# Kernel tuning notes

Measured on AMD Instinct MI355X. Metric: run time of the kernel, lower is better.

The kernel has to match this reference:

```python
import jax, jax.numpy as jnp
import numpy as np

T, B, C, S = 4096, 8, 512, 2048


def setup_inputs() -> dict:
    key = jax.random.key(0)
    k1, k2, k3 = jax.random.split(key, 3)
    x = jax.random.normal(k1, (T, B, C), dtype=jnp.float32)
    downsampling_mask = jax.random.uniform(k2, (B, T, S), dtype=jnp.float32)
    size_of_groups = jax.random.randint(k3, (B, S), 0, 4, dtype=jnp.int64)
    leftmost_group = jnp.zeros((1, 1, C), dtype=jnp.float32)
    return {"x": x, "downsampling_mask": downsampling_mask,
            "size_of_groups": size_of_groups, "leftmost_group": leftmost_group}


def reference(x, downsampling_mask, size_of_groups, leftmost_group):
    # mode == 'average': masked grouped pooling as a dense contraction
    # x: [T,B,C], mask: [B,T,S] -> downsampled: [S,B,C]
    downsampled = jnp.einsum('tbc,bts->sbc', x, downsampling_mask)
    # prepend learned leftmost group embedding, broadcast over batch
    left = jnp.broadcast_to(leftmost_group, (1, x.shape[1], x.shape[2]))
    return jnp.concatenate([left, downsampled], axis=0)  # [S+1, B, C]
```

## Files before the change

### kernel.cpp

```cpp
#include <hip/hip_runtime.h>
#include <hip/hip_bf16.h>

constexpr int T  = 4096;
constexpr int Bb = 8;
constexpr int C  = 512;
constexpr int S  = 2048;
constexpr int BC = Bb * C;

constexpr int BK = 64;
constexpr int NK = T / BK;

typedef __bf16 bf16x8 __attribute__((ext_vector_type(8)));
typedef float  f32x16 __attribute__((ext_vector_type(16)));
typedef float  f32x4  __attribute__((ext_vector_type(4)));

__device__ inline unsigned pk2(float lo, float hi) {
    union { __hip_bfloat16 h; unsigned short u; } a, b;
    a.h = __float2bfloat16(lo);
    b.h = __float2bfloat16(hi);
    return ((unsigned)b.u << 16) | (unsigned)a.u;
}

__device__ inline int slot16(int s) { return s ^ ((s >> 2) & 7); }

__global__ void left_fill(const float* __restrict__ left, float* __restrict__ out) {
    int i = blockIdx.x * blockDim.x + threadIdx.x;
    if (i < BC) out[i] = left[i & (C - 1)];
}

__global__ __launch_bounds__(512, 4) void ds_gemm(
    const float* __restrict__ x,
    const float* __restrict__ mask,
    float* __restrict__ out)
{
    __shared__ __align__(16) unsigned char smem[65536];

    const int bid0 = blockIdx.x;
    const int xcd  = bid0 & 7;
    const int slot = bid0 >> 3;
    const int b    = xcd;
    const int mt   = slot & 15;
    const int nt   = (slot >> 4) & 3;

    const int tid  = threadIdx.x;
    const int lane = tid & 63;
    const int wave = tid >> 6;
    const int h    = wave >> 2;
    const int wq   = wave & 3;
    const int wm = wq >> 1;
    const int wn = wq & 1;
    const int lm = lane & 31;
    const int kg = lane >> 5;

    const int  ii  = tid & 255;
    const int  sg  = ii & 31;
    const int  tg  = ii >> 5;
    const bool stB = (tid >= 256);

    const float* gsrc = stB
        ? x    + (size_t)(tg * 8) * BC + b * C + nt * 128 + sg * 4
        : mask + (size_t)b * T * S + (size_t)(tg * 8) * S + mt * 128 + sg * 4;
    const size_t grow  = stB ? (size_t)BC : (size_t)S;
    const size_t gstep = grow * BK;

    int waddr[4];
#pragma unroll
    for (int j = 0; j < 4; ++j)
        waddr[j] = (stB ? 16384 : 0) + tg * 2048 + slot16(sg * 4 + j) * 16;

    int raddrA[2][2], raddrB[2][2];
#pragma unroll
    for (int kk = 0; kk < 2; ++kk)
#pragma unroll
        for (int q = 0; q < 2; ++q) {
            const int oct = h * 4 + kk * 2 + kg;
            raddrA[kk][q] = oct * 2048 + slot16(wm * 64 + q * 32 + lm) * 16;
            raddrB[kk][q] = 16384 + oct * 2048 + slot16(wn * 64 + q * 32 + lm) * 16;
        }

    f32x16 acc[2][2] = {};
    f32x4  L[8];

#define LOAD_TILE(k)                                                        \
    {                                                                       \
        const float* p_ = gsrc + (size_t)(k) * gstep;                       \
        _Pragma("unroll") for (int r = 0; r < 8; ++r)                       \
            L[r] = *(const f32x4*)(p_ + (size_t)r * grow);                  \
    }

#define WRITE_TILE(buf)                                                     \
    {                                                                       \
        const int boff_ = (buf) * 32768;                                    \
        _Pragma("unroll") for (int j = 0; j < 4; ++j) {                     \
            uint4 w_;                                                       \
            w_.x = pk2(L[0][j], L[1][j]);                                   \
            w_.y = pk2(L[2][j], L[3][j]);                                   \
            w_.z = pk2(L[4][j], L[5][j]);                                   \
            w_.w = pk2(L[6][j], L[7][j]);                                   \
            *(uint4*)(smem + boff_ + waddr[j]) = w_;                        \
        }                                                                   \
    }

#define COMPUTE(buf)                                                        \
    {                                                                       \
        const int boff_ = (buf) * 32768;                                    \
        _Pragma("unroll") for (int kk = 0; kk < 2; ++kk) {                  \
            bf16x8 a0_ = *(const bf16x8*)(smem + boff_ + raddrA[kk][0]);    \
            bf16x8 a1_ = *(const bf16x8*)(smem + boff_ + raddrA[kk][1]);    \
            bf16x8 b0_ = *(const bf16x8*)(smem + boff_ + raddrB[kk][0]);    \
            bf16x8 b1_ = *(const bf16x8*)(smem + boff_ + raddrB[kk][1]);    \
            acc[0][0] = __builtin_amdgcn_mfma_f32_32x32x16_bf16(a0_, b0_, acc[0][0], 0, 0, 0); \
            acc[0][1] = __builtin_amdgcn_mfma_f32_32x32x16_bf16(a0_, b1_, acc[0][1], 0, 0, 0); \
            acc[1][0] = __builtin_amdgcn_mfma_f32_32x32x16_bf16(a1_, b0_, acc[1][0], 0, 0, 0); \
            acc[1][1] = __builtin_amdgcn_mfma_f32_32x32x16_bf16(a1_, b1_, acc[1][1], 0, 0, 0); \
        }                                                                   \
    }

    LOAD_TILE(0);

    for (int k = 0; k < NK; ++k) {
        WRITE_TILE(k & 1);
        if (k + 1 < NK) LOAD_TILE(k + 1);
        asm volatile("s_waitcnt lgkmcnt(0)" ::: "memory");
        __builtin_amdgcn_s_barrier();
        __builtin_amdgcn_sched_barrier(0);
        COMPUTE(k & 1);
    }

#undef LOAD_TILE
#undef WRITE_TILE
#undef COMPUTE

    __syncthreads();
    if (h == 1) {
#pragma unroll
        for (int m2 = 0; m2 < 2; ++m2)
#pragma unroll
            for (int n2 = 0; n2 < 2; ++n2) {
                unsigned char* base = smem + (wave - 4) * 16384 + (m2 * 2 + n2) * 4096 + lane * 16;
#pragma unroll
                for (int r4 = 0; r4 < 4; ++r4) {
                    f32x4 v = { acc[m2][n2][r4 * 4 + 0], acc[m2][n2][r4 * 4 + 1],
                                acc[m2][n2][r4 * 4 + 2], acc[m2][n2][r4 * 4 + 3] };
                    *(f32x4*)(base + r4 * 1024) = v;
                }
            }
    }
    __syncthreads();
    if (h == 0) {
#pragma unroll
        for (int m2 = 0; m2 < 2; ++m2)
#pragma unroll
            for (int n2 = 0; n2 < 2; ++n2) {
                const unsigned char* base = smem + wave * 16384 + (m2 * 2 + n2) * 4096 + lane * 16;
#pragma unroll
                for (int r4 = 0; r4 < 4; ++r4) {
                    f32x4 v = *(const f32x4*)(base + r4 * 1024);
#pragma unroll
                    for (int j = 0; j < 4; ++j) acc[m2][n2][r4 * 4 + j] += v[j];
                }
            }

        const int s_w = mt * 128 + wm * 64;
        const int c_w = nt * 128 + wn * 64;
        float* outp = out + BC;
#pragma unroll
        for (int m2 = 0; m2 < 2; ++m2)
#pragma unroll
            for (int n2 = 0; n2 < 2; ++n2)
#pragma unroll
                for (int r = 0; r < 16; ++r) {
                    const int row  = (r & 3) + 8 * (r >> 2) + 4 * kg;
                    const int srow = s_w + m2 * 32 + row;
                    const int ccol = c_w + n2 * 32 + lm;
                    outp[(size_t)srow * BC + b * C + ccol] = acc[m2][n2][r];
                }
    }
}

extern "C" void kernel_launch(void* const* d_in, const int* in_sizes, int n_in,
                              void* d_out, int out_size, void* d_ws, size_t ws_size,
                              hipStream_t stream) {
    const float* x    = (const float*)d_in[0];
    const float* mask = (const float*)d_in[1];
    const float* left = (const float*)d_in[3];
    float* out = (float*)d_out;

    left_fill<<<BC / 256, 256, 0, stream>>>(left, out);
    ds_gemm<<<Bb * (S / 128) * (C / 128), 512, 0, stream>>>(x, mask, out);
}
```

Before: 143.6 us.

## Interleave half-tile global loads and LDS writes with MFMA clusters

Restructures the main K loop so the next tile's global loads are issued before compute. Each K tile is split into two MFMA clusters, and each half of the next tile's LDS writes goes in after a partial vmcnt wait. The aim is to hide global-load latency and LDS write time behind MFMA work. It also raises wave priority around the MFMA issue with s_setprio. The cost is extra barriers per iteration (one inside each cluster plus the end-of-iteration one), more synchronisation overhead, and narrower uint2 LDS stores.

After: 155.6 us. 8.4% more time.

```diff
diff --git a/kernel.cpp b/kernel.cpp
--- a/kernel.cpp
+++ b/kernel.cpp
@@ -81,55 +81,75 @@
     f32x16 acc[2][2] = {};
     f32x4  L[8];
 
-#define LOAD_TILE(k)                                                        \
+#define LOAD_HALF(k, r0)                                                    \
     {                                                                       \
         const float* p_ = gsrc + (size_t)(k) * gstep;                       \
-        _Pragma("unroll") for (int r = 0; r < 8; ++r)                       \
-            L[r] = *(const f32x4*)(p_ + (size_t)r * grow);                  \
-    }
-
-#define WRITE_TILE(buf)                                                     \
+        _Pragma("unroll") for (int r = 0; r < 4; ++r)                       \
+            L[r0 + r] = *(const f32x4*)(p_ + (size_t)(r0 + r) * grow);      \
+    }
+
+#define WRITE_HALF(buf, r0)                                                 \
     {                                                                       \
         const int boff_ = (buf) * 32768;                                    \
         _Pragma("unroll") for (int j = 0; j < 4; ++j) {                     \
-            uint4 w_;                                                       \
-            w_.x = pk2(L[0][j], L[1][j]);                                   \
-            w_.y = pk2(L[2][j], L[3][j]);                                   \
-            w_.z = pk2(L[4][j], L[5][j]);                                   \
-            w_.w = pk2(L[6][j], L[7][j]);                                   \
-            *(uint4*)(smem + boff_ + waddr[j]) = w_;                        \
+            uint2 w_;                                                       \
+            w_.x = pk2(L[r0 + 0][j], L[r0 + 1][j]);                         \
+            w_.y = pk2(L[r0 + 2][j], L[r0 + 3][j]);                         \
+            *(uint2*)(smem + boff_ + waddr[j] + (r0 ? 8 : 0)) = w_;         \
         }                                                                   \
     }
 
-#define COMPUTE(buf)                                                        \
+#define MFMA_CLUSTER(buf, kk)                                               \
     {                                                                       \
         const int boff_ = (buf) * 32768;                                    \
-        _Pragma("unroll") for (int kk = 0; kk < 2; ++kk) {                  \
-            bf16x8 a0_ = *(const bf16x8*)(smem + boff_ + raddrA[kk][0]);    \
-            bf16x8 a1_ = *(const bf16x8*)(smem + boff_ + raddrA[kk][1]);    \
-            bf16x8 b0_ = *(const bf16x8*)(smem + boff_ + raddrB[kk][0]);    \
-            bf16x8 b1_ = *(const bf16x8*)(smem + boff_ + raddrB[kk][1]);    \
-            acc[0][0] = __builtin_amdgcn_mfma_f32_32x32x16_bf16(a0_, b0_, acc[0][0], 0, 0, 0); \
-            acc[0][1] = __builtin_amdgcn_mfma_f32_32x32x16_bf16(a0_, b1_, acc[0][1], 0, 0, 0); \
-            acc[1][0] = __builtin_amdgcn_mfma_f32_32x32x16_bf16(a1_, b0_, acc[1][0], 0, 0, 0); \
-            acc[1][1] = __builtin_amdgcn_mfma_f32_32x32x16_bf16(a1_, b1_, acc[1][1], 0, 0, 0); \
-        }                                                                   \
-    }
-
-    LOAD_TILE(0);
+        bf16x8 a0_ = *(const bf16x8*)(smem + boff_ + raddrA[kk][0]);        \
+        bf16x8 a1_ = *(const bf16x8*)(smem + boff_ + raddrA[kk][1]);        \
+        bf16x8 b0_ = *(const bf16x8*)(smem + boff_ + raddrB[kk][0]);        \
+        bf16x8 b1_ = *(const bf16x8*)(smem + boff_ + raddrB[kk][1]);        \
+        asm volatile("s_waitcnt lgkmcnt(0)" ::: "memory");                  \
+        __builtin_amdgcn_sched_barrier(0);                                  \
+        __builtin_amdgcn_s_barrier();                                       \
+        __builtin_amdgcn_sched_barrier(0);                                  \
+        __builtin_amdgcn_s_setprio(1);                                      \
+        acc[0][0] = __builtin_amdgcn_mfma_f32_32x32x16_bf16(a0_, b0_, acc[0][0], 0, 0, 0); \
+        acc[0][1] = __builtin_amdgcn_mfma_f32_32x32x16_bf16(a0_, b1_, acc[0][1], 0, 0, 0); \
+        acc[1][0] = __builtin_amdgcn_mfma_f32_32x32x16_bf16(a1_, b0_, acc[1][0], 0, 0, 0); \
+        acc[1][1] = __builtin_amdgcn_mfma_f32_32x32x16_bf16(a1_, b1_, acc[1][1], 0, 0, 0); \
+        __builtin_amdgcn_s_setprio(0);                                      \
+    }
+
+    LOAD_HALF(0, 0); LOAD_HALF(0, 4);
+    WRITE_HALF(0, 0); WRITE_HALF(0, 4);
+    asm volatile("s_waitcnt lgkmcnt(0)" ::: "memory");
+    __builtin_amdgcn_s_barrier();
+    __builtin_amdgcn_sched_barrier(0);
 
     for (int k = 0; k < NK; ++k) {
-        WRITE_TILE(k & 1);
-        if (k + 1 < NK) LOAD_TILE(k + 1);
+        const int cur = k & 1, nxt = cur ^ 1;
+        const bool pre = (k + 1 < NK);
+
+        if (pre) { LOAD_HALF(k + 1, 0); LOAD_HALF(k + 1, 4); }
+        MFMA_CLUSTER(cur, 0);
+        if (pre) {
+            asm volatile("s_waitcnt vmcnt(4)" ::: "memory");
+            __builtin_amdgcn_sched_barrier(0);
+            WRITE_HALF(nxt, 0);
+        }
+
+        MFMA_CLUSTER(cur, 1);
+        if (pre) {
+            asm volatile("s_waitcnt vmcnt(0)" ::: "memory");
+            __builtin_amdgcn_sched_barrier(0);
+            WRITE_HALF(nxt, 4);
+        }
         asm volatile("s_waitcnt lgkmcnt(0)" ::: "memory");
         __builtin_amdgcn_s_barrier();
         __builtin_amdgcn_sched_barrier(0);
-        COMPUTE(k & 1);
-    }
-
-#undef LOAD_TILE
-#undef WRITE_TILE
-#undef COMPUTE
+    }
+
+#undef LOAD_HALF
+#undef WRITE_HALF
+#undef MFMA_CLUSTER
 
     __syncthreads();
     if (h == 1) {
```
